# Kernel optimization log

Hardware: AMD Instinct MI355X
Metric: run time of the kernel (lower is better)

## Reference

```python
import jax, jax.numpy as jnp
import numpy as np

OBS_DIM = 1024
HEADS = 16
SCALE = OBS_DIM ** (-0.5)  # note: full obs_dim, as in the original module


def setup_inputs() -> dict:
    key = jax.random.key(0)
    k1, k2, k3, k4 = jax.random.split(key, 4)
    x = jax.random.normal(k1, (4, 2048, OBS_DIM), dtype=jnp.float32)
    # torch nn.Linear weight layout: [out_features, in_features]
    w_qkv = jax.random.normal(k2, (3 * OBS_DIM, OBS_DIM), dtype=jnp.float32) * (OBS_DIM ** -0.5)
    w_out = jax.random.normal(k3, (OBS_DIM, OBS_DIM), dtype=jnp.float32) * (OBS_DIM ** -0.5)
    b_out = jax.random.normal(k4, (OBS_DIM,), dtype=jnp.float32) * 0.02
    return {"x": x, "w_qkv": w_qkv, "w_out": w_out, "b_out": b_out}


def reference(x, w_qkv, w_out, b_out):
    b, n, dm = x.shape
    h = HEADS
    d = dm // h
    qkv = x @ w_qkv.T  # [b, n, 3*dm]
    # rearrange 'b n (c h d) -> c b h n d'
    qkv = qkv.reshape(b, n, 3, h, d)
    q = jnp.transpose(qkv[:, :, 0], (0, 2, 1, 3))  # [b,h,n,d]
    k = jnp.transpose(qkv[:, :, 1], (0, 2, 1, 3))
    v = jnp.transpose(qkv[:, :, 2], (0, 2, 1, 3))
    scores = jnp.einsum('bhid,bhjd->bhij', q, k) * SCALE
    att = jax.nn.softmax(scores, axis=-1)
    ctx = jnp.einsum('bhij,bhjd->bhid', att, v)  # [b,h,n,d]
    ctx = jnp.transpose(ctx, (0, 2, 1, 3)).reshape(b, n, dm)
    return ctx @ w_out.T + b_out
```

## Files before the change

kernel.cpp:

```cpp
#include <hip/hip_runtime.h>
#include <hip/hip_bf16.h>


typedef __attribute__((ext_vector_type(8))) short short8;
typedef __attribute__((ext_vector_type(4))) float float4x;
typedef __attribute__((ext_vector_type(2))) unsigned uint2x;

#define QS 8388608

#if __has_builtin(__builtin_amdgcn_exp2f)
#define FASTEXP(x) __builtin_amdgcn_exp2f(x)
#define QPRESCALE 0.0450842203f
#else
#define FASTEXP(x) __expf(x)
#define QPRESCALE 0.03125f
#endif

static __device__ __forceinline__ float4x mfma32(short8 a, short8 b, float4x c) {
    return __builtin_amdgcn_mfma_f32_16x16x32_bf16(a, b, c, 0, 0, 0);
}

static __device__ __forceinline__ void pl32swap(unsigned &a, unsigned &b) {
#if __has_builtin(__builtin_amdgcn_permlane32_swap)
    uint2x r = __builtin_amdgcn_permlane32_swap(a, b, false, false);
    a = r[0]; b = r[1];
#else
    asm("v_permlane32_swap_b32 %0, %1" : "+v"(a), "+v"(b));
#endif
}
static __device__ __forceinline__ void pl16swap(unsigned &a, unsigned &b) {
#if __has_builtin(__builtin_amdgcn_permlane16_swap)
    uint2x r = __builtin_amdgcn_permlane16_swap(a, b, false, false);
    a = r[0]; b = r[1];
#else
    asm("v_permlane16_swap_b32 %0, %1" : "+v"(a), "+v"(b));
#endif
}

static __device__ __forceinline__ short f2bf(float f) {
    union { float f; unsigned u; } x; x.f = f;
    unsigned r = x.u + 0x7fffu + ((x.u >> 16) & 1u);
    return (short)(r >> 16);
}
static __device__ __forceinline__ unsigned pack2(float a, float b) {
    return (unsigned)(unsigned short)f2bf(a) | ((unsigned)(unsigned short)f2bf(b) << 16);
}
static __device__ __forceinline__ unsigned fbits(float f) {
    union { float f; unsigned u; } x; x.f = f; return x.u;
}
static __device__ __forceinline__ unsigned permpack(float lo, float hi) {
    return __builtin_amdgcn_perm(fbits(hi), fbits(lo), 0x07060302u);
}
static __device__ __forceinline__ void async16(const void* g, void* l) {
    __builtin_amdgcn_global_load_lds(
        (const __attribute__((address_space(1))) void*)g,
        (__attribute__((address_space(3))) void*)l, 16, 0, 0);
}

__global__ __launch_bounds__(256) void cast_kernel(
    const float* __restrict__ x, const float* __restrict__ wq, const float* __restrict__ wo,
    short* __restrict__ xo, short* __restrict__ wqo, short* __restrict__ woo)
{
    int i = blockIdx.x * 256 + threadIdx.x;
    const float* src; short* dst; int off;
    if (i < 2097152)      { src = x;  dst = xo;  off = i; }
    else if (i < 2883584) { src = wq; dst = wqo; off = i - 2097152; }
    else                  { src = wo; dst = woo; off = i - 2883584; }
    float4 v = *(const float4*)(src + (size_t)off * 4);
    unsigned t[2] = {pack2(v.x, v.y), pack2(v.z, v.w)};
    *(uint2*)(dst + (size_t)off * 4) = *(uint2*)t;
}

template<int MODE>
__global__ __launch_bounds__(256) void gemm_bt_kernel(
    const short* __restrict__ A, const short* __restrict__ W,
    const float* __restrict__ bias, void* __restrict__ outp,
    int M, int N, int K)
{
    __shared__ short sh[32768];
    short* const A0 = sh;
    short* const W0 = sh + 8192;
    short* const A1 = sh + 16384;
    short* const W1 = sh + 24576;

    const int tid  = threadIdx.x;
    const int lane = tid & 63;
    const int wave = tid >> 6;
    const int row16 = lane & 15;
    const int quad  = lane >> 4;
    const int wm = wave >> 1, wn = wave & 1;

    const int l  = blockIdx.y * 64 + blockIdx.x;
    const int xcd = l & 7, s = l >> 3;
    const int m0 = (xcd * 8 + (s & 7)) * 128;
    const int n0 = (s >> 3) * 128;

    float4x acc[4][4] = {};

    auto stageAW = [&](int kb, short* Ad, short* Wd) {
        for (int r = 0; r < 4; r++) {
            int i = r * 256 + tid, row = i >> 3, cc = i & 7, sc = cc ^ (row & 7);
            async16(A + (size_t)(m0 + row) * K + kb + sc * 8, Ad + i * 8);
        }
        for (int r = 0; r < 4; r++) {
            int i = r * 256 + tid, row = i >> 3, cc = i & 7, sc = cc ^ (row & 7);
            async16(W + (size_t)(n0 + row) * K + kb + sc * 8, Wd + i * 8);
        }
    };

    stageAW(0, A0, W0);
    __syncthreads();
    const int KI = K >> 6;
    for (int ki = 0; ki < KI; ki++) {
        short* const Ac = (ki & 1) ? A1 : A0;
        short* const Wc = (ki & 1) ? W1 : W0;
        short* const An = (ki & 1) ? A0 : A1;
        short* const Wn = (ki & 1) ? W0 : W1;
        if (ki + 1 < KI) stageAW((ki + 1) << 6, An, Wn);

        short8 af[4][2], bfr[4][2];
        for (int mt = 0; mt < 4; mt++)
            for (int h = 0; h < 2; h++) {
                int row = wm * 64 + mt * 16 + row16;
                af[mt][h] = *(const short8*)&Ac[row * 64 + (((h << 2) | quad) ^ (row & 7)) * 8];
            }
        for (int nt = 0; nt < 4; nt++)
            for (int h = 0; h < 2; h++) {
                int row = wn * 64 + nt * 16 + row16;
                bfr[nt][h] = *(const short8*)&Wc[row * 64 + (((h << 2) | quad) ^ (row & 7)) * 8];
            }
        for (int mt = 0; mt < 4; mt++)
            for (int nt = 0; nt < 4; nt++) {
                acc[mt][nt] = __builtin_amdgcn_mfma_f32_16x16x32_bf16(af[mt][0], bfr[nt][0], acc[mt][nt], 0, 0, 0);
                acc[mt][nt] = __builtin_amdgcn_mfma_f32_16x16x32_bf16(af[mt][1], bfr[nt][1], acc[mt][nt], 0, 0, 0);
            }
        __syncthreads();
    }

    if (MODE == 0) {
        for (int mt = 0; mt < 4; mt++)
            for (int nt = 0; nt < 4; nt++)
                for (int r = 0; r < 4; r++) {
                    int mm = m0 + wm * 64 + mt * 16 + quad * 4 + r;
                    int nn = n0 + wn * 64 + nt * 16 + row16;
                    ((float*)outp)[(size_t)mm * N + nn] = acc[mt][nt][r] + bias[nn];
                }
    } else {
        const int c  = n0 >> 10;
        const int bb = m0 >> 11;
        for (int nt = 0; nt < 4; nt++) {
            const int rem = (n0 & 1023) + wn * 64 + nt * 16 + row16;
            const int hh = rem >> 6, dd = rem & 63;
            for (int mt = 0; mt < 4; mt++) {
                const int nsq0 = (m0 & 2047) + wm * 64 + mt * 16 + quad * 4;
                if (c == 2) {
                    size_t off = 2 * (size_t)QS + (((size_t)(bb * 16 + hh) * 64 + dd) * 2048 + nsq0);
                    uint2 w;
                    w.x = pack2(acc[mt][nt][0], acc[mt][nt][1]);
                    w.y = pack2(acc[mt][nt][2], acc[mt][nt][3]);
                    *(uint2*)((short*)outp + off) = w;
                } else {
                    size_t off = (size_t)c * QS + (((size_t)(bb * 16 + hh) * 2048 + nsq0) * 64 + dd);
                    const float scl = (c == 0) ? QPRESCALE : 1.f;
                    for (int r = 0; r < 4; r++)
                        ((short*)outp)[off + (size_t)r * 64] = f2bf(acc[mt][nt][r] * scl);
                }
            }
        }
    }
}

static __device__ __forceinline__ void stage_kv(
    const short* __restrict__ Km, const short* __restrict__ VT,
    size_t basekq, size_t basev, int kt, short* k_dst, short* v_dst, int tid)
{
    for (int r = 0; r < 2; r++) {
        int i = r * 256 + tid, row = i >> 3, cc = i & 7, sc = cc ^ (row & 7);
        async16(Km + basekq + (size_t)(kt * 64 + row) * 64 + sc * 8, k_dst + i * 8);
    }
    for (int r = 0; r < 2; r++) {
        int i = r * 256 + tid, row = i >> 3, cc = i & 7, sc = cc ^ (row & 7);
        async16(VT + basev + (size_t)row * 2048 + kt * 64 + sc * 8, v_dst + i * 8);
    }
}

__global__ __launch_bounds__(256, 2) void flash_kernel(
    const short* __restrict__ Q, const short* __restrict__ Km,
    const short* __restrict__ VT, short* __restrict__ ctx)
{
    __shared__ __align__(16) short sh[16384];

    const int id = blockIdx.y * 8 + blockIdx.x;
    const int bh = ((id & 7) << 3) | ((id >> 3) & 7);
    const int qt = id >> 6;

    const int tid  = threadIdx.x;
    const int wave = tid >> 6;
    const int lane = tid & 63;
    const int row16 = lane & 15;
    const int quad  = lane >> 4;
    const size_t basekq = (size_t)bh * 2048 * 64;
    const size_t basev  = (size_t)bh * 64 * 2048;

    short* const bufA = sh;
    short* const bufB = sh + 8192;

    short8 q[4][2];
    {
        const int qrow0 = qt * 256 + wave * 64 + row16;
        for (int u = 0; u < 4; u++)
            for (int h = 0; h < 2; h++)
                q[u][h] = *(const short8*)(Q + basekq
                            + (size_t)(qrow0 + u * 16) * 64 + (size_t)(((h << 2) | quad)) * 8);
    }
    stage_kv(Km, VT, basekq, basev, 0, bufB, bufB + 4096, tid);
    __syncthreads();

    float4x accO[4][4] = {};
    float lsum[4] = {0.f, 0.f, 0.f, 0.f};

    for (int kt = 0; kt < 32; kt++) {
        short* const cur = (kt & 1) ? bufA : bufB;
        short* const nxt = (kt & 1) ? bufB : bufA;
        if (kt < 31)
            stage_kv(Km, VT, basekq, basev, kt + 1, nxt, nxt + 4096, tid);

        short8 kf[4][2], vf[4][2];
        for (int jt = 0; jt < 4; jt++)
            for (int h = 0; h < 2; h++) {
                int row = jt * 16 + row16;
                int sl = ((((h << 2) | quad) ^ (row & 7))) * 8;
                kf[jt][h] = *(const short8*)&cur[row * 64 + sl];
                vf[jt][h] = *(const short8*)&cur[4096 + row * 64 + sl];
            }

        for (int u = 0; u < 4; u++) {
            float4x sf[4];
            for (int jt = 0; jt < 4; jt++) {
                float4x s0 = {};
                s0 = mfma32(kf[jt][0], q[u][0], s0);
                s0 = mfma32(kf[jt][1], q[u][1], s0);
                sf[jt] = s0;
            }
            unsigned wA[4][2];
            for (int jt = 0; jt < 4; jt++) {
                float e0 = FASTEXP(sf[jt][0]), e1 = FASTEXP(sf[jt][1]);
                float e2 = FASTEXP(sf[jt][2]), e3 = FASTEXP(sf[jt][3]);
                lsum[u] += (e0 + e1) + (e2 + e3);
                wA[jt][0] = permpack(e0, e1);
                wA[jt][1] = permpack(e2, e3);
            }
            short8 pf[2];
            for (int jp = 0; jp < 2; jp++) {
                unsigned a0 = wA[jp * 2][0], b0 = wA[jp * 2 + 1][0];
                unsigned a1 = wA[jp * 2][1], b1 = wA[jp * 2 + 1][1];
                pl32swap(a0, b0); pl16swap(a0, b0);
                pl32swap(a1, b1); pl16swap(a1, b1);
                union { unsigned w[4]; short8 s; } pk;
                pk.w[0] = a0; pk.w[1] = a1; pk.w[2] = b0; pk.w[3] = b1;
                pf[jp] = pk.s;
            }
            for (int dt = 0; dt < 4; dt++) {
                accO[u][dt] = mfma32(vf[dt][0], pf[0], accO[u][dt]);
                accO[u][dt] = mfma32(vf[dt][1], pf[1], accO[u][dt]);
            }
        }
        __syncthreads();
    }

    const int bb = bh >> 4, hh = bh & 15;
    for (int u = 0; u < 4; u++) {
        float l = lsum[u];
        l += __shfl_xor(l, 16);
        l += __shfl_xor(l, 32);
        const float inv = 1.f / l;
        const int nrow = qt * 256 + wave * 64 + u * 16 + row16;
        for (int dt = 0; dt < 4; dt++) {
            uint2 w;
            w.x = pack2(accO[u][dt][0] * inv, accO[u][dt][1] * inv);
            w.y = pack2(accO[u][dt][2] * inv, accO[u][dt][3] * inv);
            *(uint2*)(ctx + (size_t)(bb * 2048 + nrow) * 1024 + hh * 64 + dt * 16 + quad * 4) = w;
        }
    }
}

extern "C" void kernel_launch(void* const* d_in, const int* in_sizes, int n_in,
                              void* d_out, int out_size, void* d_ws, size_t ws_size,
                              hipStream_t stream) {
    const float* x     = (const float*)d_in[0];
    const float* w_qkv = (const float*)d_in[1];
    const float* w_out = (const float*)d_in[2];
    const float* b_out = (const float*)d_in[3];
    float* out = (float*)d_out;
    short* ws  = (short*)d_ws;

    short* qkv_ws  = ws;
    short* xbf     = ws + (size_t)3 * QS;
    short* ctx_ws  = xbf;
    short* wqkv_bf = ws + (size_t)4 * QS;
    short* wout_bf = wqkv_bf + 3145728;

    dim3 blk(256);
    cast_kernel<<<12288, blk, 0, stream>>>(x, w_qkv, w_out, xbf, wqkv_bf, wout_bf);
    gemm_bt_kernel<1><<<dim3(64, 24), blk, 0, stream>>>(xbf, wqkv_bf, nullptr, qkv_ws,
                                                        8192, 3072, 1024);
    flash_kernel<<<dim3(8, 64), blk, 0, stream>>>(qkv_ws, qkv_ws + QS, qkv_ws + 2 * (size_t)QS,
                                                  ctx_ws);
    gemm_bt_kernel<0><<<dim3(64, 8), blk, 0, stream>>>(ctx_ws, wout_bf, b_out, out,
                                                       8192, 1024, 1024);
}
```

Measured before the change: 239.8 us.

## Software-pipeline QK^T MFMAs ahead of softmax in flash loop with priority hints

Restructures the flash attention inner loop so the QK^T MFMAs for the next 16-row query sub-tile are issued before the exp/pack work of the current sub-tile. This lets matrix ops overlap with transcendental and permute work. It also precomputes staging pointers and LDS offsets so per-iteration address arithmetic is reduced, and adds s_setprio around MFMA groups. The cost is higher register pressure from keeping two score tiles live under a 2-blocks-per-SM launch bound.

```diff
diff --git a/kernel.cpp b/kernel.cpp
--- a/kernel.cpp
+++ b/kernel.cpp
@@ -170,20 +170,6 @@
     }
 }
 
-static __device__ __forceinline__ void stage_kv(
-    const short* __restrict__ Km, const short* __restrict__ VT,
-    size_t basekq, size_t basev, int kt, short* k_dst, short* v_dst, int tid)
-{
-    for (int r = 0; r < 2; r++) {
-        int i = r * 256 + tid, row = i >> 3, cc = i & 7, sc = cc ^ (row & 7);
-        async16(Km + basekq + (size_t)(kt * 64 + row) * 64 + sc * 8, k_dst + i * 8);
-    }
-    for (int r = 0; r < 2; r++) {
-        int i = r * 256 + tid, row = i >> 3, cc = i & 7, sc = cc ^ (row & 7);
-        async16(VT + basev + (size_t)row * 2048 + kt * 64 + sc * 8, v_dst + i * 8);
-    }
-}
-
 __global__ __launch_bounds__(256, 2) void flash_kernel(
     const short* __restrict__ Q, const short* __restrict__ Km,
     const short* __restrict__ VT, short* __restrict__ ctx)
@@ -213,56 +199,95 @@
                 q[u][h] = *(const short8*)(Q + basekq
                             + (size_t)(qrow0 + u * 16) * 64 + (size_t)(((h << 2) | quad)) * 8);
     }
-    stage_kv(Km, VT, basekq, basev, 0, bufB, bufB + 4096, tid);
+
+    const int srow = tid >> 3;
+    const int ssc  = ((tid & 7) ^ (srow & 7)) * 8;
+    const short* gk  = Km + basekq + (size_t)srow * 64 + ssc;
+    const short* gk2 = gk + 2048;
+    const short* gv  = VT + basev + (size_t)srow * 2048 + ssc;
+    const short* gv2 = gv + 65536;
+    const int ldst = tid * 8;
+
+    const int koff0 = row16 * 64 + ((quad ^ (row16 & 7))) * 8;
+    const int koff1 = row16 * 64 + (((4 | quad) ^ (row16 & 7))) * 8;
+
+    async16(gk,  bufB + ldst);        async16(gk2, bufB + ldst + 2048);
+    async16(gv,  bufB + 4096 + ldst); async16(gv2, bufB + 4096 + ldst + 2048);
+    gk += 4096; gk2 += 4096; gv += 64; gv2 += 64;
     __syncthreads();
 
     float4x accO[4][4] = {};
     float lsum[4] = {0.f, 0.f, 0.f, 0.f};
+    const float4x FZ = {};
 
     for (int kt = 0; kt < 32; kt++) {
         short* const cur = (kt & 1) ? bufA : bufB;
         short* const nxt = (kt & 1) ? bufB : bufA;
-        if (kt < 31)
-            stage_kv(Km, VT, basekq, basev, kt + 1, nxt, nxt + 4096, tid);
-
+        if (kt < 31) {
+            async16(gk,  nxt + ldst);        async16(gk2, nxt + ldst + 2048);
+            async16(gv,  nxt + 4096 + ldst); async16(gv2, nxt + 4096 + ldst + 2048);
+            gk += 4096; gk2 += 4096; gv += 64; gv2 += 64;
+        }
+
+        const short* b0 = cur + koff0;
+        const short* b1 = cur + koff1;
         short8 kf[4][2], vf[4][2];
-        for (int jt = 0; jt < 4; jt++)
-            for (int h = 0; h < 2; h++) {
-                int row = jt * 16 + row16;
-                int sl = ((((h << 2) | quad) ^ (row & 7))) * 8;
-                kf[jt][h] = *(const short8*)&cur[row * 64 + sl];
-                vf[jt][h] = *(const short8*)&cur[4096 + row * 64 + sl];
-            }
-
+#pragma unroll
+        for (int jt = 0; jt < 4; jt++) {
+            kf[jt][0] = *(const short8*)(b0 + jt * 1024);
+            kf[jt][1] = *(const short8*)(b1 + jt * 1024);
+            vf[jt][0] = *(const short8*)(b0 + 4096 + jt * 1024);
+            vf[jt][1] = *(const short8*)(b1 + 4096 + jt * 1024);
+        }
+
+        float4x sfA[4];
+        __builtin_amdgcn_s_setprio(1);
+#pragma unroll
+        for (int jt = 0; jt < 4; jt++) {
+            float4x s0 = mfma32(kf[jt][0], q[0][0], FZ);
+            sfA[jt] = mfma32(kf[jt][1], q[0][1], s0);
+        }
+        __builtin_amdgcn_s_setprio(0);
+
+#pragma unroll
         for (int u = 0; u < 4; u++) {
-            float4x sf[4];
-            for (int jt = 0; jt < 4; jt++) {
-                float4x s0 = {};
-                s0 = mfma32(kf[jt][0], q[u][0], s0);
-                s0 = mfma32(kf[jt][1], q[u][1], s0);
-                sf[jt] = s0;
-            }
-            unsigned wA[4][2];
-            for (int jt = 0; jt < 4; jt++) {
-                float e0 = FASTEXP(sf[jt][0]), e1 = FASTEXP(sf[jt][1]);
-                float e2 = FASTEXP(sf[jt][2]), e3 = FASTEXP(sf[jt][3]);
-                lsum[u] += (e0 + e1) + (e2 + e3);
-                wA[jt][0] = permpack(e0, e1);
-                wA[jt][1] = permpack(e2, e3);
+            float4x sfB[4];
+            if (u < 3) {
+                __builtin_amdgcn_s_setprio(1);
+#pragma unroll
+                for (int jt = 0; jt < 4; jt++) {
+                    float4x s0 = mfma32(kf[jt][0], q[u + 1][0], FZ);
+                    sfB[jt] = mfma32(kf[jt][1], q[u + 1][1], s0);
+                }
+                __builtin_amdgcn_s_setprio(0);
             }
             short8 pf[2];
+#pragma unroll
             for (int jp = 0; jp < 2; jp++) {
-                unsigned a0 = wA[jp * 2][0], b0 = wA[jp * 2 + 1][0];
-                unsigned a1 = wA[jp * 2][1], b1 = wA[jp * 2 + 1][1];
-                pl32swap(a0, b0); pl16swap(a0, b0);
-                pl32swap(a1, b1); pl16swap(a1, b1);
+                float4x sa = sfA[jp * 2], sb = sfA[jp * 2 + 1];
+                float a0 = FASTEXP(sa[0]), a1 = FASTEXP(sa[1]);
+                float a2 = FASTEXP(sa[2]), a3 = FASTEXP(sa[3]);
+                float b0e = FASTEXP(sb[0]), b1e = FASTEXP(sb[1]);
+                float b2e = FASTEXP(sb[2]), b3e = FASTEXP(sb[3]);
+                lsum[u] += ((a0 + a1) + (a2 + a3)) + ((b0e + b1e) + (b2e + b3e));
+                unsigned wa0 = permpack(a0, a1), wa1 = permpack(a2, a3);
+                unsigned wb0 = permpack(b0e, b1e), wb1 = permpack(b2e, b3e);
+                pl32swap(wa0, wb0); pl16swap(wa0, wb0);
+                pl32swap(wa1, wb1); pl16swap(wa1, wb1);
                 union { unsigned w[4]; short8 s; } pk;
-                pk.w[0] = a0; pk.w[1] = a1; pk.w[2] = b0; pk.w[3] = b1;
+                pk.w[0] = wa0; pk.w[1] = wa1; pk.w[2] = wb0; pk.w[3] = wb1;
                 pf[jp] = pk.s;
             }
+            __builtin_amdgcn_s_setprio(1);
+#pragma unroll
             for (int dt = 0; dt < 4; dt++) {
                 accO[u][dt] = mfma32(vf[dt][0], pf[0], accO[u][dt]);
                 accO[u][dt] = mfma32(vf[dt][1], pf[1], accO[u][dt]);
+            }
+            __builtin_amdgcn_s_setprio(0);
+            if (u < 3) {
+#pragma unroll
+                for (int jt = 0; jt < 4; jt++) sfA[jt] = sfB[jt];
             }
         }
         __syncthreads();
```

After: 234.7 us. -2.1%, faster.
